# Kernel tuning notes

Hardware: AMD Instinct MI355X
Metric: run time of the kernel (lower is better)

Reference implementation:

```python
import jax, jax.numpy as jnp
import numpy as np

K_MIN = 30.0
TAU = 1e-06
BETA = 0.9
LAMBDA_MAX = 0.1
LAMBDA_SCALE = 1.0

N, D_OUT, N_MODULES, N_CONTEXTS = 262144, 128, 64, 16


def setup_inputs() -> dict:
    key = jax.random.key(0)
    k1, k2, k3, k4 = jax.random.split(key, 4)
    Y_hat = jax.random.normal(k1, (N, D_OUT), dtype=jnp.float32)
    context_weights = jax.random.uniform(k2, (N, N_CONTEXTS), dtype=jnp.float32)
    M_pinv = jax.random.normal(k3, (N_MODULES, D_OUT), dtype=jnp.float32) * 0.1
    C_prior = jax.random.normal(k4, (N_CONTEXTS, N_MODULES, N_MODULES), dtype=jnp.float32) * 0.1
    # Buffers exactly as registered in __init__
    ema_Sigma = jnp.broadcast_to(jnp.eye(N_MODULES, dtype=jnp.float32), (N_CONTEXTS, N_MODULES, N_MODULES))
    ema_sigma_sq = jnp.ones((N_CONTEXTS, N_MODULES), dtype=jnp.float32)
    ema_initialized = jnp.zeros((N_CONTEXTS,), dtype=bool)
    return {"Y_hat": Y_hat, "context_weights": context_weights, "M_pinv": M_pinv,
            "C_prior": C_prior, "ema_Sigma": ema_Sigma, "ema_sigma_sq": ema_sigma_sq,
            "ema_initialized": ema_initialized}


def reference(Y_hat, context_weights, M_pinv, C_prior, ema_Sigma, ema_sigma_sq, ema_initialized):
    # Z_hat: [N, m]
    Z = Y_hat @ M_pinv.T
    wsum = context_weights.sum(axis=0)            # [T] == eff_n per context
    active = wsum >= K_MIN                        # context skipping, vectorized
    # Weighted mean per context: [T, m]
    mu = (context_weights.T @ Z) / wsum[:, None]
    # Weighted covariance: sum_n w_norm * (z-mu)(z-mu)^T == E_w[zz^T] - mu mu^T
    w_norm = context_weights / wsum[None, :]      # [N, T]
    S = jnp.einsum('nt,nm,nk->tmk', w_norm, Z, Z)  # [T, m, m]
    Sigma = S - mu[:, :, None] * mu[:, None, :]
    # EMA sigma_sq update (no-grad in original -> stop_gradient)
    Sigma_sg = jax.lax.stop_gradient(Sigma)
    diag_init = jnp.diagonal(Sigma_sg, axis1=1, axis2=2)                       # first-call branch
    diag_ema = jnp.diagonal(BETA * ema_Sigma + (1.0 - BETA) * Sigma_sg, axis1=1, axis2=2)
    sigma_sq = jnp.where(ema_initialized[:, None], diag_ema, diag_init)        # [T, m]
    std = jnp.sqrt(sigma_sq + TAU)
    denom = std[:, :, None] * std[:, None, :]
    C_hat = jnp.clip(Sigma / (denom + TAU), -1.0, 1.0)
    loss_t = jnp.sum((C_hat - C_prior) ** 2, axis=(1, 2)) / wsum               # [T]
    n_active = jnp.sum(active)
    total = jnp.sum(jnp.where(active, loss_t, 0.0))
    total = jnp.where(n_active > 0,
                      LAMBDA_MAX * LAMBDA_SCALE * total / jnp.maximum(n_active, 1).astype(total.dtype),
                      jnp.zeros((), total.dtype))
    return total
```

## Files before the change

kernel.cpp:

```cpp
#include <hip/hip_runtime.h>
#include <stdint.h>

#define N_ROWS 262144
#define D_OUTC 128
#define M_MOD  64
#define T_CTX  16

#define ZB_OFF   ((size_t)0)
#define ZB_BYTES ((size_t)M_MOD * N_ROWS * 2)
#define WT_OFF   (ZB_OFF + ZB_BYTES)
#define WT_BYTES ((size_t)T_CTX * N_ROWS * 2)
#define SS_OFF   (WT_OFF + WT_BYTES)
#define SS_BYTES ((size_t)T_CTX * M_MOD * M_MOD * 4)
#define B_OFF    (SS_OFF + SS_BYTES)
#define B_BYTES  ((size_t)T_CTX * M_MOD * 4)
#define WSUM_OFF (B_OFF + B_BYTES)
#define WSUM_BYTES ((size_t)64)
#define LT_OFF   (WSUM_OFF + WSUM_BYTES)
#define LT_BYTES ((size_t)64)
#define PSS_OFF  (LT_OFF + LT_BYTES)
#define PSS_BYTES ((size_t)256 * T_CTX * M_MOD * M_MOD * 2)
#define NEED_BIG (PSS_OFF + PSS_BYTES)

typedef __attribute__((ext_vector_type(4))) float f32x4;
typedef __attribute__((ext_vector_type(8))) _Float16 f16x8;
typedef __attribute__((ext_vector_type(2))) _Float16 h2;

union FR { uint4 u; f16x8 v; h2 h[4]; };

__device__ __forceinline__ float bf2f(unsigned short u) {
  return __uint_as_float(((unsigned int)u) << 16);
}
__device__ __forceinline__ unsigned short f2bf(float f) {
  unsigned int x = __float_as_uint(f);
  return (unsigned short)((x + 0x7fffu + ((x >> 16) & 1u)) >> 16);
}
__device__ __forceinline__ h2 cvt_pkrtz(float a, float b) {
  return __builtin_bit_cast(h2, __builtin_amdgcn_cvt_pkrtz(a, b));
}
#if __has_builtin(__builtin_amdgcn_fdot2)
__device__ __forceinline__ float fdot2f(h2 a, h2 b, float c) {
  return __builtin_amdgcn_fdot2(a, b, c, false);
}
#else
__device__ __forceinline__ float fdot2f(h2 a, h2 b, float c) {
  return c + (float)a[0] * (float)b[0] + (float)a[1] * (float)b[1];
}
#endif

#define WAITVM(N) asm volatile("s_waitcnt vmcnt(" #N ")" ::: "memory")
#define SBAR() do { __builtin_amdgcn_s_barrier(); __builtin_amdgcn_sched_barrier(0); } while (0)

__global__ __launch_bounds__(256) void wtr_kernel(const float* __restrict__ W,
                                                  _Float16* __restrict__ Wt)
{
  __shared__ float Wf[16][260];
  const int tid = threadIdx.x;
  const int n0  = blockIdx.x * 256;
  {
    const float4* src = (const float4*)(W + (size_t)(n0 + tid) * T_CTX);
#pragma unroll
    for (int q = 0; q < 4; ++q) {
      float4 v = src[q];
      Wf[q * 4 + 0][tid] = v.x; Wf[q * 4 + 1][tid] = v.y;
      Wf[q * 4 + 2][tid] = v.z; Wf[q * 4 + 3][tid] = v.w;
    }
  }
  __syncthreads();
  const int t = tid >> 4, c0 = (tid & 15) * 16;
  FR o[2];
#pragma unroll
  for (int j = 0; j < 2; ++j)
#pragma unroll
    for (int p = 0; p < 4; ++p)
      o[j].h[p] = cvt_pkrtz(Wf[t][c0 + j * 8 + 2 * p], Wf[t][c0 + j * 8 + 2 * p + 1]);
  uint4* dst = (uint4*)(Wt + (size_t)t * N_ROWS + n0 + c0);
  dst[0] = o[0].u; dst[1] = o[1].u;
}

__global__ __launch_bounds__(256, 6) void zk_kernel(
    const float* __restrict__ Y, const float* __restrict__ Mp,
    _Float16* __restrict__ Zbt)
{
  __shared__ __align__(16) _Float16 Mpl[64 * 128];
  const int tid = threadIdx.x;
  const int l   = tid & 63;
  const int wv  = tid >> 6;
  const int g   = l >> 4;
  const int col = l & 15;
  {
    const int m  = tid >> 2;
    const int dq = tid & 3;
#pragma unroll
    for (int i = 0; i < 4; ++i) {
      const int s = dq * 4 + i;
      const float* mp = Mp + (size_t)m * D_OUTC + s * 8;
      float4 a = *(const float4*)mp;
      float4 b = *(const float4*)(mp + 4);
      FR o;
      o.h[0] = cvt_pkrtz(a.x, a.y); o.h[1] = cvt_pkrtz(a.z, a.w);
      o.h[2] = cvt_pkrtz(b.x, b.y); o.h[3] = cvt_pkrtz(b.z, b.w);
      const int ss = (s & ~7) | ((s & 7) ^ (m & 7));
      *(uint4*)((char*)&Mpl[0] + m * 256 + ss * 16) = o.u;
    }
  }
  __syncthreads();
#pragma unroll
  for (int it = 0; it < 2; ++it) {
    const int n0 = (blockIdx.x * 2 + it) * 64;
    const int nr = n0 + wv * 16 + col;
    const float* __restrict__ yr = Y + (size_t)nr * D_OUTC;
    float4 yv[8];
#pragma unroll
    for (int ks = 0; ks < 4; ++ks) {
      yv[2 * ks]     = *(const float4*)(yr + ks * 32 + g * 8);
      yv[2 * ks + 1] = *(const float4*)(yr + ks * 32 + g * 8 + 4);
    }
    f32x4 acc[4];
#pragma unroll
    for (int qi = 0; qi < 4; ++qi) acc[qi] = (f32x4){0.f, 0.f, 0.f, 0.f};
#pragma unroll
    for (int ks = 0; ks < 4; ++ks) {
      const float* f0 = (const float*)&yv[2 * ks];
      const float* f1 = (const float*)&yv[2 * ks + 1];
      FR B;
      B.h[0] = cvt_pkrtz(f0[0], f0[1]); B.h[1] = cvt_pkrtz(f0[2], f0[3]);
      B.h[2] = cvt_pkrtz(f1[0], f1[1]); B.h[3] = cvt_pkrtz(f1[2], f1[3]);
#pragma unroll
      for (int qi = 0; qi < 4; ++qi) {
        const int m = qi * 16 + col;
        const int s = ks * 4 + g;
        FR A;
        A.u = *(const uint4*)((char*)&Mpl[0] + m * 256 + 16 * ((s & ~7) | ((s & 7) ^ (m & 7))));
        acc[qi] = __builtin_amdgcn_mfma_f32_16x16x32_f16(A.v, B.v, acc[qi], 0, 0, 0);
      }
    }
#pragma unroll
    for (int qi = 0; qi < 4; ++qi)
#pragma unroll
      for (int i = 0; i < 4; ++i)
        Zbt[(size_t)(qi * 16 + g * 4 + i) * N_ROWS + n0 + wv * 16 + col] =
            (_Float16)acc[qi][i];
  }
}

#define SS_NS 256
#define NCH   16
template <bool PARTIAL>
__global__ __launch_bounds__(512, 4) void ss_kernel(
    const _Float16* __restrict__ Zbt, const _Float16* __restrict__ Wt,
    float* __restrict__ SS, float* __restrict__ Bm,
    unsigned short* __restrict__ Pss)
{
  __shared__ __align__(16) _Float16 Zl[4][64 * 64];
  __shared__ __align__(16) _Float16 Wlds[8 * 1024];
  const int tid = threadIdx.x;
  const int l   = tid & 63;
  const int wv  = tid >> 6;
  const int g   = l >> 4;
  const int col = l & 15;
  const int ns  = blockIdx.x & (SS_NS - 1);
  const int cg  = blockIdx.x >> 8;
  const int ctx = cg * 8 + wv;
  const int n0b = ns * 1024;

  f32x4 acc[4][4];
  f32x4 accB[4];
#pragma unroll
  for (int a = 0; a < 4; ++a) {
    accB[a] = (f32x4){0.f, 0.f, 0.f, 0.f};
#pragma unroll
    for (int b = 0; b < 4; ++b) acc[a][b] = (f32x4){0.f, 0.f, 0.f, 0.f};
  }
  FR ones;
#pragma unroll
  for (int j = 0; j < 4; ++j) ones.h[j] = (h2){(_Float16)1.f, (_Float16)1.f};

#pragma unroll
  for (int k = 0; k < 2; ++k) {
    const _Float16* wsrc = Wt + (size_t)ctx * N_ROWS + n0b + k * 512 + l * 8;
    __builtin_amdgcn_global_load_lds((const unsigned int*)wsrc,
        (unsigned int*)((char*)&Wlds[0] + wv * 2048 + k * 1024), 16, 0, 0);
  }
  const int zrow  = 8 * wv + (l >> 3);
  const int zslot = l & 7;
  auto stage = [&](int c) {
    const int n0 = n0b + c * 64;
    const _Float16* src = Zbt + (size_t)zrow * N_ROWS + n0 + 8 * (zslot ^ (zrow & 7));
    __builtin_amdgcn_global_load_lds((const unsigned int*)src,
        (unsigned int*)((char*)&Zl[c & 3][0] + wv * 1024 + l * 16), 16, 0, 0);
  };

  stage(0); stage(1); stage(2);
  WAITVM(2);
  SBAR();

  for (int c = 0; c < NCH; ++c) {
    if (c + 3 < NCH) stage(c + 3);
    const char* zb = (const char*)&Zl[c & 3][0];
    const char* wb = (const char*)&Wlds[0] + wv * 2048 + c * 128;
#pragma unroll
    for (int s = 0; s < 2; ++s) {
      FR wfr;
      wfr.u = *(const uint4*)(wb + s * 64 + g * 16);
      FR fr[4];
#pragma unroll
      for (int qi = 0; qi < 4; ++qi) {
        const int r = qi * 16 + col;
        fr[qi].u = *(const uint4*)(zb + r * 128 + 16 * ((s * 4 + g) ^ (r & 7)));
      }
      __builtin_amdgcn_s_setprio(1);
#pragma unroll
      for (int qi = 0; qi < 4; ++qi) {
        FR A;
#pragma unroll
        for (int j = 0; j < 4; ++j) A.h[j] = fr[qi].h[j] * wfr.h[j];
        accB[qi] = __builtin_amdgcn_mfma_f32_16x16x32_f16(A.v, ones.v, accB[qi], 0, 0, 0);
#pragma unroll
        for (int ki = 0; ki < 4; ++ki)
          acc[qi][ki] = __builtin_amdgcn_mfma_f32_16x16x32_f16(A.v, fr[ki].v, acc[qi][ki], 0, 0, 0);
      }
      __builtin_amdgcn_s_setprio(0);
    }
    if (c + 3 < NCH)       { WAITVM(2); SBAR(); }
    else if (c == NCH - 3) { WAITVM(1); SBAR(); }
    else if (c == NCH - 2) { WAITVM(0); SBAR(); }
  }

  if (col == 0) {
#pragma unroll
    for (int qi = 0; qi < 4; ++qi)
#pragma unroll
      for (int i = 0; i < 4; ++i)
        atomicAdd(&Bm[ctx * 64 + qi * 16 + g * 4 + i], accB[qi][i]);
  }
  if (PARTIAL) {
    unsigned short* P = Pss + ((size_t)ns * 16 + ctx) * 4096;
#pragma unroll
    for (int qi = 0; qi < 4; ++qi)
#pragma unroll
      for (int ki = 0; ki < 4; ++ki)
#pragma unroll
        for (int i = 0; i < 4; ++i)
          P[(qi * 16 + g * 4 + i) * 64 + ki * 16 + col] = f2bf(acc[qi][ki][i]);
  } else {
#pragma unroll
    for (int qi = 0; qi < 4; ++qi)
#pragma unroll
      for (int ki = 0; ki < 4; ++ki)
#pragma unroll
        for (int i = 0; i < 4; ++i)
          atomicAdd(&SS[(size_t)ctx * 4096 + (qi * 16 + g * 4 + i) * 64 + ki * 16 + col],
                    acc[qi][ki][i]);
  }
}

__global__ __launch_bounds__(256) void wsk_kernel(const _Float16* __restrict__ Wt,
                                                  float* __restrict__ wsum)
{
  const int tid = threadIdx.x;
  const int t = blockIdx.x >> 2, q = blockIdx.x & 3;
  const uint4* base = (const uint4*)(Wt + (size_t)t * N_ROWS + q * 65536);
  const h2 one2 = {(_Float16)1.f, (_Float16)1.f};
  float s = 0.f;
  for (int i = tid; i < 8192; i += 256) {
    uint4 v = base[i];
    const h2* h = (const h2*)&v;
#pragma unroll
    for (int j = 0; j < 4; ++j) s = fdot2f(h[j], one2, s);
  }
  s += __shfl_xor(s, 1);  s += __shfl_xor(s, 2);
  s += __shfl_xor(s, 4);  s += __shfl_xor(s, 8);
  s += __shfl_xor(s, 16); s += __shfl_xor(s, 32);
  __shared__ float red[4];
  if ((tid & 63) == 0) red[tid >> 6] = s;
  __syncthreads();
  if (tid == 0) atomicAdd(&wsum[t], red[0] + red[1] + red[2] + red[3]);
}

__global__ __launch_bounds__(256) void ssred_kernel(
    const unsigned short* __restrict__ Pss, float* __restrict__ SS)
{
  const int e = blockIdx.x * 256 + threadIdx.x;
  float s = 0.f;
#pragma unroll 8
  for (int b = 0; b < 256; ++b)
    s += bf2f(Pss[(size_t)b * 65536 + e]);
  SS[e] = s;
}

__global__ __launch_bounds__(64) void fin1_kernel(
    const float* __restrict__ SS, const float* __restrict__ Bm,
    const float* __restrict__ wsum, const float* __restrict__ Cp,
    const float* __restrict__ emaS, const unsigned char* __restrict__ inited,
    float* __restrict__ LT)
{
  const int t = blockIdx.x, m = threadIdx.x;
  __shared__ float muL[64], stdL[64];
  const float ws  = wsum[t];
  const float inv = 1.0f / ws;
  const float mu  = Bm[t * 64 + m] * inv;
  {
    float Smm = SS[(size_t)t * 4096 + m * 65] * inv - mu * mu;
    float de  = 0.9f * emaS[(size_t)t * 4096 + m * 65] + 0.1f * Smm;
    float sq  = inited[t] ? de : Smm;
    muL[m]  = mu;
    stdL[m] = sqrtf(sq + 1e-6f);
  }
  __syncthreads();
  const float sm = stdL[m];
  const float* SSr = SS + (size_t)t * 4096 + m * 64;
  const float* Cpr = Cp + (size_t)t * 4096 + m * 64;
  float acc = 0.f;
#pragma unroll
  for (int k = 0; k < 64; ++k) {
    float Sig = SSr[k] * inv - mu * muL[k];
    float den = sm * stdL[k] + 1e-6f;
    float ch  = fminf(1.f, fmaxf(-1.f, Sig / den));
    float d   = ch - Cpr[k];
    acc = fmaf(d, d, acc);
  }
#pragma unroll
  for (int o = 1; o < 64; o <<= 1) acc += __shfl_xor(acc, o);
  if (m == 0) LT[t] = acc * inv;
}

__global__ __launch_bounds__(64) void fin2_kernel(
    const float* __restrict__ LT, const float* __restrict__ wsum,
    float* __restrict__ out)
{
  const int l = threadIdx.x;
  float lt = 0.f, act = 0.f;
  if (l < 16) {
    float ws = wsum[l];
    if (ws >= 30.0f) { act = 1.f; lt = LT[l]; }
  }
#pragma unroll
  for (int o = 1; o < 16; o <<= 1) {
    lt  += __shfl_xor(lt, o);
    act += __shfl_xor(act, o);
  }
  if (l == 0) out[0] = (act > 0.f) ? (0.1f * 1.0f * lt / act) : 0.f;
}

extern "C" void kernel_launch(void* const* d_in, const int* in_sizes, int n_in,
                              void* d_out, int out_size, void* d_ws, size_t ws_size,
                              hipStream_t stream) {
  (void)in_sizes; (void)n_in; (void)out_size;
  const float* Y    = (const float*)d_in[0];
  const float* W    = (const float*)d_in[1];
  const float* Mp   = (const float*)d_in[2];
  const float* Cp   = (const float*)d_in[3];
  const float* emaS = (const float*)d_in[4];
  const unsigned char* inited = (const unsigned char*)d_in[6];
  float* out = (float*)d_out;
  char* ws = (char*)d_ws;
  _Float16* Zbt = (_Float16*)(ws + ZB_OFF);
  _Float16* Wt  = (_Float16*)(ws + WT_OFF);
  float* SS   = (float*)(ws + SS_OFF);
  float* Bm   = (float*)(ws + B_OFF);
  float* wsum = (float*)(ws + WSUM_OFF);
  float* LT   = (float*)(ws + LT_OFF);
  unsigned short* Pss = (unsigned short*)(ws + PSS_OFF);

  wtr_kernel<<<N_ROWS / 256, 256, 0, stream>>>(W, Wt);
  zk_kernel<<<N_ROWS / 128, 256, 0, stream>>>(Y, Mp, Zbt);
  if (ws_size >= NEED_BIG) {
    (void)hipMemsetAsync(ws + B_OFF, 0, B_BYTES + WSUM_BYTES, stream);
    ss_kernel<true><<<2 * SS_NS, 512, 0, stream>>>(Zbt, Wt, SS, Bm, Pss);
    wsk_kernel<<<64, 256, 0, stream>>>(Wt, wsum);
    ssred_kernel<<<256, 256, 0, stream>>>(Pss, SS);
  } else {
    (void)hipMemsetAsync(ws + SS_OFF, 0, SS_BYTES + B_BYTES + WSUM_BYTES, stream);
    ss_kernel<false><<<2 * SS_NS, 512, 0, stream>>>(Zbt, Wt, SS, Bm, Pss);
    wsk_kernel<<<64, 256, 0, stream>>>(Wt, wsum);
  }
  fin1_kernel<<<16, 64, 0, stream>>>(SS, Bm, wsum, Cp, emaS, inited, LT);
  fin2_kernel<<<1, 64, 0, stream>>>(LT, wsum, out);
}
```

Measured before the change: 139.7 us.

## Fuse weight sums into transpose kernel and restructure Z projection stores

Computes the per-context weight sums inside the weight transpose kernel, with shuffle reductions and padded atomic slots, so the separate wsum kernel and its second read of Wt go away. The Z projection kernel now issues both row tiles' Y loads before the barrier, swaps the MFMA operands so each lane writes four contiguous fp16 values as one packed store, and lowers its occupancy hint. The SS kernel's block-index mapping is interleaved so the two context groups for the same row slice run close together, which may improve L2 reuse of Z. Risks include atomic contention on wsum (1024 blocks × 16 contexts) and more register pressure in zk.

Result: slower. 144.0 us (+3.1%).

```diff
diff --git a/kernel.cpp b/kernel.cpp
--- a/kernel.cpp
+++ b/kernel.cpp
@@ -15,7 +15,7 @@
 #define B_OFF    (SS_OFF + SS_BYTES)
 #define B_BYTES  ((size_t)T_CTX * M_MOD * 4)
 #define WSUM_OFF (B_OFF + B_BYTES)
-#define WSUM_BYTES ((size_t)64)
+#define WSUM_BYTES ((size_t)1024)
 #define LT_OFF   (WSUM_OFF + WSUM_BYTES)
 #define LT_BYTES ((size_t)64)
 #define PSS_OFF  (LT_OFF + LT_BYTES)
@@ -38,21 +38,13 @@
 __device__ __forceinline__ h2 cvt_pkrtz(float a, float b) {
   return __builtin_bit_cast(h2, __builtin_amdgcn_cvt_pkrtz(a, b));
 }
-#if __has_builtin(__builtin_amdgcn_fdot2)
-__device__ __forceinline__ float fdot2f(h2 a, h2 b, float c) {
-  return __builtin_amdgcn_fdot2(a, b, c, false);
-}
-#else
-__device__ __forceinline__ float fdot2f(h2 a, h2 b, float c) {
-  return c + (float)a[0] * (float)b[0] + (float)a[1] * (float)b[1];
-}
-#endif
 
 #define WAITVM(N) asm volatile("s_waitcnt vmcnt(" #N ")" ::: "memory")
 #define SBAR() do { __builtin_amdgcn_s_barrier(); __builtin_amdgcn_sched_barrier(0); } while (0)
 
 __global__ __launch_bounds__(256) void wtr_kernel(const float* __restrict__ W,
-                                                  _Float16* __restrict__ Wt)
+                                                  _Float16* __restrict__ Wt,
+                                                  float* __restrict__ wsum)
 {
   __shared__ float Wf[16][260];
   const int tid = threadIdx.x;
@@ -69,16 +61,23 @@
   __syncthreads();
   const int t = tid >> 4, c0 = (tid & 15) * 16;
   FR o[2];
+  float s = 0.f;
 #pragma unroll
   for (int j = 0; j < 2; ++j)
 #pragma unroll
-    for (int p = 0; p < 4; ++p)
-      o[j].h[p] = cvt_pkrtz(Wf[t][c0 + j * 8 + 2 * p], Wf[t][c0 + j * 8 + 2 * p + 1]);
+    for (int p = 0; p < 4; ++p) {
+      float a = Wf[t][c0 + j * 8 + 2 * p], b = Wf[t][c0 + j * 8 + 2 * p + 1];
+      o[j].h[p] = cvt_pkrtz(a, b);
+      s += a + b;
+    }
   uint4* dst = (uint4*)(Wt + (size_t)t * N_ROWS + n0 + c0);
   dst[0] = o[0].u; dst[1] = o[1].u;
-}
-
-__global__ __launch_bounds__(256, 6) void zk_kernel(
+  s += __shfl_xor(s, 1); s += __shfl_xor(s, 2);
+  s += __shfl_xor(s, 4); s += __shfl_xor(s, 8);
+  if ((tid & 15) == 0) atomicAdd(&wsum[t * 16], s);
+}
+
+__global__ __launch_bounds__(256, 4) void zk_kernel(
     const float* __restrict__ Y, const float* __restrict__ Mp,
     _Float16* __restrict__ Zbt)
 {
@@ -88,6 +87,8 @@
   const int wv  = tid >> 6;
   const int g   = l >> 4;
   const int col = l & 15;
+  const int n0  = blockIdx.x * 128;
+
   {
     const int m  = tid >> 2;
     const int dq = tid & 3;
@@ -100,22 +101,31 @@
       FR o;
       o.h[0] = cvt_pkrtz(a.x, a.y); o.h[1] = cvt_pkrtz(a.z, a.w);
       o.h[2] = cvt_pkrtz(b.x, b.y); o.h[3] = cvt_pkrtz(b.z, b.w);
-      const int ss = (s & ~7) | ((s & 7) ^ (m & 7));
-      *(uint4*)((char*)&Mpl[0] + m * 256 + ss * 16) = o.u;
-    }
+      const int ss2 = (s & ~7) | ((s & 7) ^ (m & 7));
+      *(uint4*)((char*)Mpl + m * 256 + ss2 * 16) = o.u;
+    }
+  }
+  const int nt0 = n0 + wv * 16;
+  const int nt1 = n0 + 64 + wv * 16;
+  const float* __restrict__ yr0 = Y + (size_t)(nt0 + col) * D_OUTC;
+  const float* __restrict__ yr1 = Y + (size_t)(nt1 + col) * D_OUTC;
+  float4 yv0[8], yv1[8];
+#pragma unroll
+  for (int ks = 0; ks < 4; ++ks) {
+    yv0[2 * ks]     = *(const float4*)(yr0 + ks * 32 + g * 8);
+    yv0[2 * ks + 1] = *(const float4*)(yr0 + ks * 32 + g * 8 + 4);
+  }
+#pragma unroll
+  for (int ks = 0; ks < 4; ++ks) {
+    yv1[2 * ks]     = *(const float4*)(yr1 + ks * 32 + g * 8);
+    yv1[2 * ks + 1] = *(const float4*)(yr1 + ks * 32 + g * 8 + 4);
   }
   __syncthreads();
+
 #pragma unroll
   for (int it = 0; it < 2; ++it) {
-    const int n0 = (blockIdx.x * 2 + it) * 64;
-    const int nr = n0 + wv * 16 + col;
-    const float* __restrict__ yr = Y + (size_t)nr * D_OUTC;
-    float4 yv[8];
-#pragma unroll
-    for (int ks = 0; ks < 4; ++ks) {
-      yv[2 * ks]     = *(const float4*)(yr + ks * 32 + g * 8);
-      yv[2 * ks + 1] = *(const float4*)(yr + ks * 32 + g * 8 + 4);
-    }
+    const float4* yv = (it == 0) ? yv0 : yv1;
+    const int nt = (it == 0) ? nt0 : nt1;
     f32x4 acc[4];
 #pragma unroll
     for (int qi = 0; qi < 4; ++qi) acc[qi] = (f32x4){0.f, 0.f, 0.f, 0.f};
@@ -123,29 +133,31 @@
     for (int ks = 0; ks < 4; ++ks) {
       const float* f0 = (const float*)&yv[2 * ks];
       const float* f1 = (const float*)&yv[2 * ks + 1];
-      FR B;
-      B.h[0] = cvt_pkrtz(f0[0], f0[1]); B.h[1] = cvt_pkrtz(f0[2], f0[3]);
-      B.h[2] = cvt_pkrtz(f1[0], f1[1]); B.h[3] = cvt_pkrtz(f1[2], f1[3]);
+      FR Yf;
+      Yf.h[0] = cvt_pkrtz(f0[0], f0[1]); Yf.h[1] = cvt_pkrtz(f0[2], f0[3]);
+      Yf.h[2] = cvt_pkrtz(f1[0], f1[1]); Yf.h[3] = cvt_pkrtz(f1[2], f1[3]);
 #pragma unroll
       for (int qi = 0; qi < 4; ++qi) {
         const int m = qi * 16 + col;
         const int s = ks * 4 + g;
-        FR A;
-        A.u = *(const uint4*)((char*)&Mpl[0] + m * 256 + 16 * ((s & ~7) | ((s & 7) ^ (m & 7))));
-        acc[qi] = __builtin_amdgcn_mfma_f32_16x16x32_f16(A.v, B.v, acc[qi], 0, 0, 0);
+        FR Mf;
+        Mf.u = *(const uint4*)((char*)Mpl + m * 256 + 16 * ((s & ~7) | ((s & 7) ^ (m & 7))));
+        acc[qi] = __builtin_amdgcn_mfma_f32_16x16x32_f16(Yf.v, Mf.v, acc[qi], 0, 0, 0);
       }
     }
 #pragma unroll
-    for (int qi = 0; qi < 4; ++qi)
-#pragma unroll
-      for (int i = 0; i < 4; ++i)
-        Zbt[(size_t)(qi * 16 + g * 4 + i) * N_ROWS + n0 + wv * 16 + col] =
-            (_Float16)acc[qi][i];
-  }
-}
-
-#define SS_NS 256
-#define NCH   16
+    for (int qi = 0; qi < 4; ++qi) {
+      const int m = qi * 16 + col;
+      h2 lo, hi;
+      lo[0] = (_Float16)acc[qi][0]; lo[1] = (_Float16)acc[qi][1];
+      hi[0] = (_Float16)acc[qi][2]; hi[1] = (_Float16)acc[qi][3];
+      uint2 pk = {__builtin_bit_cast(unsigned int, lo), __builtin_bit_cast(unsigned int, hi)};
+      *(uint2*)(Zbt + (size_t)m * N_ROWS + nt + g * 4) = pk;
+    }
+  }
+}
+
+#define NCH 16
 template <bool PARTIAL>
 __global__ __launch_bounds__(512, 4) void ss_kernel(
     const _Float16* __restrict__ Zbt, const _Float16* __restrict__ Wt,
@@ -159,8 +171,9 @@
   const int wv  = tid >> 6;
   const int g   = l >> 4;
   const int col = l & 15;
-  const int ns  = blockIdx.x & (SS_NS - 1);
-  const int cg  = blockIdx.x >> 8;
+  const int x   = blockIdx.x;
+  const int cg  = (x >> 3) & 1;
+  const int ns  = (x & 7) | ((x >> 4) << 3);
   const int ctx = cg * 8 + wv;
   const int n0b = ns * 1024;
 
@@ -180,7 +193,7 @@
   for (int k = 0; k < 2; ++k) {
     const _Float16* wsrc = Wt + (size_t)ctx * N_ROWS + n0b + k * 512 + l * 8;
     __builtin_amdgcn_global_load_lds((const unsigned int*)wsrc,
-        (unsigned int*)((char*)&Wlds[0] + wv * 2048 + k * 1024), 16, 0, 0);
+        (unsigned int*)((char*)Wlds + wv * 2048 + k * 1024), 16, 0, 0);
   }
   const int zrow  = 8 * wv + (l >> 3);
   const int zslot = l & 7;
@@ -198,7 +211,7 @@
   for (int c = 0; c < NCH; ++c) {
     if (c + 3 < NCH) stage(c + 3);
     const char* zb = (const char*)&Zl[c & 3][0];
-    const char* wb = (const char*)&Wlds[0] + wv * 2048 + c * 128;
+    const char* wb = (const char*)Wlds + wv * 2048 + c * 128;
 #pragma unroll
     for (int s = 0; s < 2; ++s) {
       FR wfr;
@@ -253,29 +266,6 @@
           atomicAdd(&SS[(size_t)ctx * 4096 + (qi * 16 + g * 4 + i) * 64 + ki * 16 + col],
                     acc[qi][ki][i]);
   }
-}
-
-__global__ __launch_bounds__(256) void wsk_kernel(const _Float16* __restrict__ Wt,
-                                                  float* __restrict__ wsum)
-{
-  const int tid = threadIdx.x;
-  const int t = blockIdx.x >> 2, q = blockIdx.x & 3;
-  const uint4* base = (const uint4*)(Wt + (size_t)t * N_ROWS + q * 65536);
-  const h2 one2 = {(_Float16)1.f, (_Float16)1.f};
-  float s = 0.f;
-  for (int i = tid; i < 8192; i += 256) {
-    uint4 v = base[i];
-    const h2* h = (const h2*)&v;
-#pragma unroll
-    for (int j = 0; j < 4; ++j) s = fdot2f(h[j], one2, s);
-  }
-  s += __shfl_xor(s, 1);  s += __shfl_xor(s, 2);
-  s += __shfl_xor(s, 4);  s += __shfl_xor(s, 8);
-  s += __shfl_xor(s, 16); s += __shfl_xor(s, 32);
-  __shared__ float red[4];
-  if ((tid & 63) == 0) red[tid >> 6] = s;
-  __syncthreads();
-  if (tid == 0) atomicAdd(&wsum[t], red[0] + red[1] + red[2] + red[3]);
 }
 
 __global__ __launch_bounds__(256) void ssred_kernel(
@@ -297,7 +287,7 @@
 {
   const int t = blockIdx.x, m = threadIdx.x;
   __shared__ float muL[64], stdL[64];
-  const float ws  = wsum[t];
+  const float ws  = wsum[t * 16];
   const float inv = 1.0f / ws;
   const float mu  = Bm[t * 64 + m] * inv;
   {
@@ -332,7 +322,7 @@
   const int l = threadIdx.x;
   float lt = 0.f, act = 0.f;
   if (l < 16) {
-    float ws = wsum[l];
+    float ws = wsum[l * 16];
     if (ws >= 30.0f) { act = 1.f; lt = LT[l]; }
   }
 #pragma unroll
@@ -363,17 +353,17 @@
   float* LT   = (float*)(ws + LT_OFF);
   unsigned short* Pss = (unsigned short*)(ws + PSS_OFF);
 
-  wtr_kernel<<<N_ROWS / 256, 256, 0, stream>>>(W, Wt);
-  zk_kernel<<<N_ROWS / 128, 256, 0, stream>>>(Y, Mp, Zbt);
   if (ws_size >= NEED_BIG) {
     (void)hipMemsetAsync(ws + B_OFF, 0, B_BYTES + WSUM_BYTES, stream);
-    ss_kernel<true><<<2 * SS_NS, 512, 0, stream>>>(Zbt, Wt, SS, Bm, Pss);
-    wsk_kernel<<<64, 256, 0, stream>>>(Wt, wsum);
+    wtr_kernel<<<N_ROWS / 256, 256, 0, stream>>>(W, Wt, wsum);
+    zk_kernel<<<N_ROWS / 128, 256, 0, stream>>>(Y, Mp, Zbt);
+    ss_kernel<true><<<512, 512, 0, stream>>>(Zbt, Wt, SS, Bm, Pss);
     ssred_kernel<<<256, 256, 0, stream>>>(Pss, SS);
   } else {
     (void)hipMemsetAsync(ws + SS_OFF, 0, SS_BYTES + B_BYTES + WSUM_BYTES, stream);
-    ss_kernel<false><<<2 * SS_NS, 512, 0, stream>>>(Zbt, Wt, SS, Bm, Pss);
-    wsk_kernel<<<64, 256, 0, stream>>>(Wt, wsum);
+    wtr_kernel<<<N_ROWS / 256, 256, 0, stream>>>(W, Wt, wsum);
+    zk_kernel<<<N_ROWS / 128, 256, 0, stream>>>(Y, Mp, Zbt);
+    ss_kernel<false><<<512, 512, 0, stream>>>(Zbt, Wt, SS, Bm, Pss);
   }
   fin1_kernel<<<16, 64, 0, stream>>>(SS, Bm, wsum, Cp, emaS, inited, LT);
   fin2_kernel<<<1, 64, 0, stream>>>(LT, wsum, out);
```
